# Kernel tuning notes

Measured on AMD Instinct MI355X. Metric: run time of the kernel, lower is better.

## Reference

```python
import jax, jax.numpy as jnp
import numpy as np

NUM_E = 100000
NUM_R = 500
HIDDEN = 64
BATCH = 32
GAMMA = 12.0
EPSILON = 2.0
EMB_RANGE = (GAMMA + EPSILON) / HIDDEN  # 0.21875
PI = 3.141592653589793


def setup_inputs() -> dict:
    key = jax.random.key(0)
    k1, k2, k3 = jax.random.split(key, 3)
    facts = jax.random.randint(k1, (BATCH, 3), 0, 1000, dtype=jnp.int64)  # col0<num_e, col1<2*num_r
    entity_embedding = jax.random.uniform(
        k2, (NUM_E, 2 * HIDDEN), dtype=jnp.float32, minval=-EMB_RANGE, maxval=EMB_RANGE)
    relation_embedding = jax.random.uniform(
        k3, (NUM_R * 2, HIDDEN), dtype=jnp.float32, minval=-EMB_RANGE, maxval=EMB_RANGE)
    return {"facts": facts, "entity_embedding": entity_embedding,
            "relation_embedding": relation_embedding}


def reference(facts, entity_embedding, relation_embedding):
    # Gather head/relation embeddings for the batch
    head = entity_embedding[facts[:, 0]]          # [B, 2D]
    relation = relation_embedding[facts[:, 1]]    # [B, D]

    re_head, im_head = jnp.split(head, 2, axis=1)           # [B, D] each
    re_tail, im_tail = jnp.split(entity_embedding, 2, axis=1)  # [E, D] each

    phase = relation / (EMB_RANGE / PI)
    re_rel = jnp.cos(phase)
    im_rel = jnp.sin(phase)

    # Complex rotation of head by relation: [B, D]
    re_rot = re_head * re_rel - im_head * im_rel
    im_rot = re_head * im_rel + im_head * re_rel

    # Broadcast difference against all entities: [B, E, D]
    re_diff = re_rot[:, None, :] - re_tail[None, :, :]
    im_diff = im_rot[:, None, :] - im_tail[None, :, :]

    # Per-component complex modulus, summed over dim -> [B, E]
    dist = jnp.sqrt(re_diff * re_diff + im_diff * im_diff).sum(axis=2)
    return GAMMA - dist
```

## Files before the change

kernel.cpp:

```cpp
#include <hip/hip_runtime.h>
#include <math.h>

#define NUM_E   100000
#define HIDDEN  64
#define BATCH   32
#define GAMMA_F 12.0f
#define EMB_RANGE_F 0.21875f
#define INV_TWO_EMB (1.0f / (2.0f * EMB_RANGE_F))

typedef float v4f __attribute__((ext_vector_type(4)));

__global__ void rotate_phase_kernel(const int* __restrict__ facts,
                                    const float* __restrict__ ent,
                                    const float* __restrict__ rel,
                                    float* __restrict__ rot) {
    int p = blockIdx.x * blockDim.x + threadIdx.x;
    if (p >= BATCH * HIDDEN) return;
    int b = p >> 6;
    int d = p & 63;
    int f0 = facts[b * 3 + 0];
    int f1 = facts[b * 3 + 1];
    float hre = ent[(size_t)f0 * 128 + d];
    float him = ent[(size_t)f0 * 128 + 64 + d];
    float r   = rel[(size_t)f1 * 64 + d];
    float rev = r * INV_TWO_EMB;
    float s = __builtin_amdgcn_sinf(rev);
    float c = __builtin_amdgcn_cosf(rev);
    rot[p]                  = hre * c - him * s;
    rot[BATCH * HIDDEN + p] = hre * s + him * c;
}

__global__ __launch_bounds__(256, 4) void rotate_dist_kernel(
        const float* __restrict__ ent,
        const float* __restrict__ rot,
        float* __restrict__ out) {
    __shared__ float s_ent[32 * 128];

    const int t     = threadIdx.x;
    const int tile0 = blockIdx.x * 32;

    const int lane = t & 63;
    const int wv   = t >> 6;
    const int bg   = lane & 15;
    const int dg   = lane >> 4;
    v4f RR[2][4], RI[2][4];
#pragma unroll
    for (int kb = 0; kb < 2; ++kb) {
        const int b = bg * 2 + kb;
        const v4f* pr = (const v4f*)(rot + b * 64 + dg * 16);
        const v4f* pi = (const v4f*)(rot + 2048 + b * 64 + dg * 16);
#pragma unroll
        for (int c = 0; c < 4; ++c) { RR[kb][c] = pr[c]; RI[kb][c] = pi[c]; }
    }

    {
        const v4f* g4 = (const v4f*)(ent + (size_t)tile0 * 128);
        v4f* s4 = (v4f*)s_ent;
#pragma unroll
        for (int j = 0; j < 4; ++j) s4[t + 256 * j] = g4[t + 256 * j];
    }
    __syncthreads();

#pragma unroll 1
    for (int i = 0; i < 8; ++i) {
        const int e_local = wv * 8 + i;
        const int e       = tile0 + e_local;
        const v4f* pr = (const v4f*)(s_ent + e_local * 128 + dg * 16);
        const v4f* pi = (const v4f*)(s_ent + e_local * 128 + 64 + dg * 16);
        v4f er[4], ei[4];
#pragma unroll
        for (int c = 0; c < 4; ++c) { er[c] = pr[c]; ei[c] = pi[c]; }

        float sum0, sum1;
#pragma unroll
        for (int kb = 0; kb < 2; ++kb) {
            v4f a = (v4f){0.f, 0.f, 0.f, 0.f};
#pragma unroll
            for (int c = 0; c < 4; ++c) {
                v4f dx = RR[kb][c] - er[c];
                v4f dy = RI[kb][c] - ei[c];
                v4f s  = dx * dx + dy * dy;
                a.x += __builtin_amdgcn_sqrtf(s.x);
                a.y += __builtin_amdgcn_sqrtf(s.y);
                a.z += __builtin_amdgcn_sqrtf(s.z);
                a.w += __builtin_amdgcn_sqrtf(s.w);
            }
            float sm = (a.x + a.y) + (a.z + a.w);
            sm += __shfl_xor(sm, 16, 64);
            sm += __shfl_xor(sm, 32, 64);
            if (kb == 0) sum0 = sm; else sum1 = sm;
        }
        if (dg < 2)
            out[(size_t)(bg * 2 + dg) * NUM_E + e] =
                GAMMA_F - (dg == 0 ? sum0 : sum1);
    }
}

extern "C" void kernel_launch(void* const* d_in, const int* in_sizes, int n_in,
                              void* d_out, int out_size, void* d_ws, size_t ws_size,
                              hipStream_t stream) {
    const int*   facts = (const int*)d_in[0];
    const float* ent   = (const float*)d_in[1];
    const float* rel   = (const float*)d_in[2];
    float*       out   = (float*)d_out;
    float*       rot   = (float*)d_ws;

    rotate_phase_kernel<<<dim3((BATCH * HIDDEN + 255) / 256), dim3(256), 0, stream>>>(
        facts, ent, rel, rot);

    rotate_dist_kernel<<<dim3(NUM_E / 32), dim3(256), 0, stream>>>(
        ent, rot, out);
}
```

Before: 124.9 us.

## Remap distance kernel lanes, use packed FP32 math, DPP reductions, LDS-staged stores

```diff
diff --git a/kernel.cpp b/kernel.cpp
--- a/kernel.cpp
+++ b/kernel.cpp
@@ -9,6 +9,36 @@
 #define INV_TWO_EMB (1.0f / (2.0f * EMB_RANGE_F))
 
 typedef float v4f __attribute__((ext_vector_type(4)));
+typedef float v2f __attribute__((ext_vector_type(2)));
+
+static __device__ __forceinline__ v2f pk_sub(v2f a, v2f b) {
+    v2f d;
+    asm("v_pk_add_f32 %0, %1, %2 neg_lo:[0,1] neg_hi:[0,1]"
+        : "=v"(d) : "v"(a), "v"(b));
+    return d;
+}
+static __device__ __forceinline__ v2f pk_mul(v2f a, v2f b) {
+    v2f d;
+    asm("v_pk_mul_f32 %0, %1, %2" : "=v"(d) : "v"(a), "v"(b));
+    return d;
+}
+static __device__ __forceinline__ v2f pk_fma(v2f a, v2f b, v2f c) {
+    v2f d;
+    asm("v_pk_fma_f32 %0, %1, %2, %3" : "=v"(d) : "v"(a), "v"(b), "v"(c));
+    return d;
+}
+static __device__ __forceinline__ float sq2(v2f dx, v2f dy) {
+    v2f sq = pk_fma(dy, dy, pk_mul(dx, dx));
+    return __builtin_amdgcn_sqrtf(sq.x) + __builtin_amdgcn_sqrtf(sq.y);
+}
+static __device__ __forceinline__ v2f lo2(v4f v) { return __builtin_shufflevector(v, v, 0, 1); }
+static __device__ __forceinline__ v2f hi2(v4f v) { return __builtin_shufflevector(v, v, 2, 3); }
+
+template <int CTRL>
+static __device__ __forceinline__ float dpp_xor_add(float x) {
+    int y = __builtin_amdgcn_update_dpp(0, __float_as_int(x), CTRL, 0xF, 0xF, true);
+    return x + __int_as_float(y);
+}
 
 __global__ void rotate_phase_kernel(const int* __restrict__ facts,
                                     const float* __restrict__ ent,
@@ -34,65 +64,85 @@
         const float* __restrict__ ent,
         const float* __restrict__ rot,
         float* __restrict__ out) {
-    __shared__ float s_ent[32 * 128];
+    __shared__ float s_ent[4096];
+    __shared__ float s_scr[4][136];
 
-    const int t     = threadIdx.x;
-    const int tile0 = blockIdx.x * 32;
-
+    const int t    = threadIdx.x;
     const int lane = t & 63;
     const int wv   = t >> 6;
-    const int bg   = lane & 15;
-    const int dg   = lane >> 4;
-    v4f RR[2][4], RI[2][4];
+    const int bg   = lane >> 3;
+    const int dg   = lane & 7;
+    const int e0   = blockIdx.x * 32 + wv * 8;
+
+    v2f RR[4][4], RI[4][4];
 #pragma unroll
-    for (int kb = 0; kb < 2; ++kb) {
-        const int b = bg * 2 + kb;
-        const v4f* pr = (const v4f*)(rot + b * 64 + dg * 16);
-        const v4f* pi = (const v4f*)(rot + 2048 + b * 64 + dg * 16);
-#pragma unroll
-        for (int c = 0; c < 4; ++c) { RR[kb][c] = pr[c]; RI[kb][c] = pi[c]; }
+    for (int kb = 0; kb < 4; ++kb) {
+        const v4f* pr = (const v4f*)(rot + (bg * 4 + kb) * 64 + dg * 8);
+        const v4f* pi = (const v4f*)(rot + 2048 + (bg * 4 + kb) * 64 + dg * 8);
+        v4f a = pr[0], b = pr[1], c = pi[0], d = pi[1];
+        RR[kb][0] = lo2(a); RR[kb][1] = hi2(a); RR[kb][2] = lo2(b); RR[kb][3] = hi2(b);
+        RI[kb][0] = lo2(c); RI[kb][1] = hi2(c); RI[kb][2] = lo2(d); RI[kb][3] = hi2(d);
     }
 
+    float* lds = s_ent + wv * 1024;
     {
-        const v4f* g4 = (const v4f*)(ent + (size_t)tile0 * 128);
-        v4f* s4 = (v4f*)s_ent;
+        const v4f* g4 = (const v4f*)(ent + (size_t)e0 * 128);
+        v4f* s4 = (v4f*)lds;
 #pragma unroll
-        for (int j = 0; j < 4; ++j) s4[t + 256 * j] = g4[t + 256 * j];
+        for (int k = 0; k < 4; ++k) s4[k * 64 + lane] = g4[k * 64 + lane];
     }
-    __syncthreads();
+
+    float* scr = s_scr[wv];
 
 #pragma unroll 1
-    for (int i = 0; i < 8; ++i) {
-        const int e_local = wv * 8 + i;
-        const int e       = tile0 + e_local;
-        const v4f* pr = (const v4f*)(s_ent + e_local * 128 + dg * 16);
-        const v4f* pi = (const v4f*)(s_ent + e_local * 128 + 64 + dg * 16);
-        v4f er[4], ei[4];
+    for (int grp = 0; grp < 2; ++grp) {
+        float p[4][4];
+
 #pragma unroll
-        for (int c = 0; c < 4; ++c) { er[c] = pr[c]; ei[c] = pi[c]; }
+        for (int i = 0; i < 4; ++i) {
+            const float* base = lds + (grp * 4 + i) * 128 + dg * 8;
+            v4f er0 = *(const v4f*)(base);
+            v4f er1 = *(const v4f*)(base + 4);
+            v4f ei0 = *(const v4f*)(base + 64);
+            v4f ei1 = *(const v4f*)(base + 68);
+            v2f e2[4] = { lo2(er0), hi2(er0), lo2(er1), hi2(er1) };
+            v2f i2[4] = { lo2(ei0), hi2(ei0), lo2(ei1), hi2(ei1) };
+#pragma unroll
+            for (int kb = 0; kb < 4; ++kb) {
+                float s0 = sq2(pk_sub(RR[kb][0], e2[0]), pk_sub(RI[kb][0], i2[0]));
+                float s1 = sq2(pk_sub(RR[kb][1], e2[1]), pk_sub(RI[kb][1], i2[1]));
+                float s2 = sq2(pk_sub(RR[kb][2], e2[2]), pk_sub(RI[kb][2], i2[2]));
+                float s3 = sq2(pk_sub(RR[kb][3], e2[3]), pk_sub(RI[kb][3], i2[3]));
+                p[i][kb] = (s0 + s1) + (s2 + s3);
+            }
+        }
 
-        float sum0, sum1;
 #pragma unroll
-        for (int kb = 0; kb < 2; ++kb) {
-            v4f a = (v4f){0.f, 0.f, 0.f, 0.f};
+        for (int i = 0; i < 4; ++i)
 #pragma unroll
-            for (int c = 0; c < 4; ++c) {
-                v4f dx = RR[kb][c] - er[c];
-                v4f dy = RI[kb][c] - ei[c];
-                v4f s  = dx * dx + dy * dy;
-                a.x += __builtin_amdgcn_sqrtf(s.x);
-                a.y += __builtin_amdgcn_sqrtf(s.y);
-                a.z += __builtin_amdgcn_sqrtf(s.z);
-                a.w += __builtin_amdgcn_sqrtf(s.w);
+            for (int kb = 0; kb < 4; ++kb) {
+                float v = p[i][kb];
+                v = dpp_xor_add<0xB1>(v);
+                v = dpp_xor_add<0x4E>(v);
+                v += __shfl_xor(v, 4, 64);
+                p[i][kb] = GAMMA_F - v;
             }
-            float sm = (a.x + a.y) + (a.z + a.w);
-            sm += __shfl_xor(sm, 16, 64);
-            sm += __shfl_xor(sm, 32, 64);
-            if (kb == 0) sum0 = sm; else sum1 = sm;
+
+        if (dg < 4) {
+#pragma unroll
+            for (int i = 0; i < 4; ++i) {
+                float val = (dg == 0) ? p[i][0] : (dg == 1) ? p[i][1]
+                          : (dg == 2) ? p[i][2] : p[i][3];
+                scr[i * 33 + bg * 4 + dg] = val;
+            }
         }
-        if (dg < 2)
-            out[(size_t)(bg * 2 + dg) * NUM_E + e] =
-                GAMMA_F - (dg == 0 ? sum0 : sum1);
+#pragma unroll
+        for (int j = 0; j < 2; ++j) {
+            const int b  = (lane >> 2) + 16 * j;
+            const int el = lane & 3;
+            float v = scr[el * 33 + b];
+            out[(size_t)b * NUM_E + e0 + grp * 4 + el] = v;
+        }
     }
 }
 
```

Result: faster. 118.4 us (-5.1%).
